# Optimization experiments

Hardware: AMD Instinct MI355X
Metric: run time of the kernel (lower is better)

The kernel has to match this reference:

```python
import jax, jax.numpy as jnp
import numpy as np

B, D, M = 32, 640, 1024
EPS = 1e-05


def setup_inputs() -> dict:
    key = jax.random.key(0)
    x = jax.random.normal(key, (B, D, M), dtype=jnp.float32)
    return {"x": x}


def _triu_flat_indices(d):
    iu, ju = np.triu_indices(d)
    return jnp.asarray(iu * d + ju, dtype=jnp.int32)


def reference(x):
    b, d, m = x.shape
    # Gram matrix: x @ x^T  -> [b, d, d]
    x_pow2 = jnp.einsum('bim,bjm->bij', x, x)
    # I_M @ (x_pow2 * I) + (x_pow2 * I) @ I_M - 2*x_pow2
    # (x_pow2 * I) is diagonal, so ones-matrix bmm = broadcast of the diagonal.
    diag = jnp.diagonal(x_pow2, axis1=1, axis2=2)  # [b, d]
    dcov = diag[:, None, :] + diag[:, :, None] - 2.0 * x_pow2
    dcov = jnp.maximum(dcov, 0.0)
    # temperature param is built in-forward: exp(log(1/(2*d*m))) = 1/(2*d*m)
    temperature = 1.0 / (2.0 * d * m)
    dcov = jnp.sqrt(temperature * dcov + EPS)
    # Double centering: dcov @ I_M = row sums broadcast; I_M @ dcov = col sums.
    row_mean = dcov.sum(axis=2, keepdims=True) / d          # [b, d, 1]
    col_mean = dcov.sum(axis=1, keepdims=True) / d          # [b, 1, d]
    tot_mean = dcov.sum(axis=(1, 2), keepdims=True) / (d * d)
    t = dcov - row_mean - col_mean + tot_mean               # [b, d, d]
    # Triuvec: gather upper-triangular entries (incl. diagonal)
    flat_idx = _triu_flat_indices(d)                         # [d*(d+1)//2]
    y = t.reshape(b, d * d)[:, flat_idx]
    return y
```

## Files before the change

kernel.cpp:

```cpp
#include <hip/hip_runtime.h>

#define D_DIM 640
#define M_DIM 1024
#define B_DIM 32
#define BK 32
#define OUT_ROW 205120

typedef __bf16 bf16x8 __attribute__((ext_vector_type(8)));
typedef float f32x4 __attribute__((ext_vector_type(4)));

__device__ __forceinline__ unsigned short f2bf(float f) {
    union { float f; unsigned int u; } c; c.f = f;
    unsigned int u = c.u;
    unsigned int r = (u + 0x7fffu + ((u >> 16) & 1u)) >> 16;
    return (unsigned short)r;
}

__device__ __forceinline__ void gload_lds16(const unsigned short* g, unsigned short* l) {
    __builtin_amdgcn_global_load_lds(
        (const __attribute__((address_space(1))) unsigned int*)g,
        (__attribute__((address_space(3))) unsigned int*)l,
        16, 0, 0);
}

__device__ __forceinline__ float block_reduce_256(float s) {
    #pragma unroll
    for (int off = 32; off > 0; off >>= 1) s += __shfl_down(s, off, 64);
    __shared__ float red[4];
    if ((threadIdx.x & 63) == 0) red[threadIdx.x >> 6] = s;
    __syncthreads();
    return red[0] + red[1] + red[2] + red[3];
}

__global__ void cast_diag_kernel(const float* __restrict__ x,
                                 unsigned short* __restrict__ xb,
                                 float* __restrict__ diag,
                                 float* __restrict__ rowsum,
                                 float* __restrict__ tot) {
    const size_t row = blockIdx.x;
    const int t = threadIdx.x;
    const float4 v = ((const float4*)(x + row * M_DIM))[t];
    float s = v.x * v.x + v.y * v.y + v.z * v.z + v.w * v.w;
    ushort4 o;
    o.x = f2bf(v.x); o.y = f2bf(v.y); o.z = f2bf(v.z); o.w = f2bf(v.w);
    ((ushort4*)(xb + row * M_DIM))[t] = o;
    float ssum = block_reduce_256(s);
    if (t == 0) { diag[row] = ssum; rowsum[row] = 0.f; }
    if (t == 1 && row < B_DIM) tot[row] = 0.f;
}

__global__ __launch_bounds__(256, 2)
void gemm_dcov_kernel(const unsigned short* __restrict__ xb,
                      const float* __restrict__ diag,
                      float* __restrict__ dcov,
                      float* __restrict__ rowsum,
                      float* __restrict__ tot) {
    __shared__ __align__(16) unsigned short smem[2 * 128 * BK];
    unsigned short* sA = smem;
    unsigned short* sB = smem + 128 * BK;

    int p = blockIdx.x, bt = blockIdx.y;
    int it = 0, off = p;
    while (off >= 5 - it) { off -= 5 - it; ++it; }
    const int jt = it + off;
    const bool diagTile = (it == jt);

    const int tid = threadIdx.x;
    const int w = tid >> 6, l = tid & 63;
    const int wy = w >> 1, wx = w & 1;
    const int lm = l & 15, quad = l >> 4;

    const unsigned short* gA = xb + ((size_t)bt * D_DIM + it * 128) * M_DIM;
    const unsigned short* gB = xb + ((size_t)bt * D_DIM + jt * 128) * M_DIM;

    const int r0 = tid >> 2;
    const int cl = (((tid & 3) ^ ((tid >> 3) & 3)) << 3);
    const size_t aoff1 = (size_t)r0 * M_DIM + cl;
    const size_t aoff2 = (size_t)(r0 + 64) * M_DIM + cl;
    const int ldst = tid * 8;

    f32x4 acc[4][4];
    const f32x4 zero = {0.f, 0.f, 0.f, 0.f};
    #pragma unroll
    for (int i = 0; i < 4; i++)
        #pragma unroll
        for (int j = 0; j < 4; j++) acc[i][j] = zero;

    const int sw = ((quad ^ ((lm >> 1) & 3)) << 3);

    for (int k0 = 0; k0 < M_DIM; k0 += BK) {
        gload_lds16(gA + aoff1 + k0, sA + ldst);
        gload_lds16(gA + aoff2 + k0, sA + ldst + 64 * BK);
        if (!diagTile) {
            gload_lds16(gB + aoff1 + k0, sB + ldst);
            gload_lds16(gB + aoff2 + k0, sB + ldst + 64 * BK);
        }
        __syncthreads();

        const unsigned short* sBB = diagTile ? sA : sB;
        bf16x8 af[4], bfr[4];
        #pragma unroll
        for (int mi = 0; mi < 4; mi++)
            af[mi] = *(const bf16x8*)&sA[(wy * 64 + mi * 16 + lm) * BK + sw];
        #pragma unroll
        for (int ni = 0; ni < 4; ni++)
            bfr[ni] = *(const bf16x8*)&sBB[(wx * 64 + ni * 16 + lm) * BK + sw];

        #pragma unroll
        for (int mi = 0; mi < 4; mi++)
            #pragma unroll
            for (int ni = 0; ni < 4; ni++)
                acc[mi][ni] = __builtin_amdgcn_mfma_f32_16x16x32_bf16(
                    af[mi], bfr[ni], acc[mi][ni], 0, 0, 0);
        __syncthreads();
    }

    float* sd = (float*)smem;
    if (tid < 128) sd[tid] = diag[(size_t)bt * D_DIM + it * 128 + tid];
    else           sd[tid] = diag[(size_t)bt * D_DIM + jt * 128 + (tid - 128)];
    __syncthreads();

    const float temp = 7.62939453125e-07f;
    float* dbase = dcov + (size_t)bt * D_DIM * D_DIM;
    float* rs = rowsum + (size_t)bt * D_DIM;
    float ts = 0.f;
    float cp[4] = {0.f, 0.f, 0.f, 0.f};

    #pragma unroll
    for (int mi = 0; mi < 4; mi++) {
        #pragma unroll
        for (int r = 0; r < 4; r++) {
            const int lrow = wy * 64 + mi * 16 + quad * 4 + r;
            const int grow = it * 128 + lrow;
            const float di = sd[lrow];
            float rp = 0.f;
            #pragma unroll
            for (int ni = 0; ni < 4; ni++) {
                const int lcol = wx * 64 + ni * 16 + lm;
                const int gcol = jt * 128 + lcol;
                const float dj = sd[128 + lcol];
                const float g = acc[mi][ni][r];
                const float v = sqrtf(fmaf(temp, fmaxf(di + dj - 2.f * g, 0.f), 1e-5f));
                dbase[(size_t)grow * D_DIM + gcol] = v;
                rp += v;
                cp[ni] += v;
            }
            ts += rp;
            rp += __shfl_down(rp, 8, 16);
            rp += __shfl_down(rp, 4, 16);
            rp += __shfl_down(rp, 2, 16);
            rp += __shfl_down(rp, 1, 16);
            if (lm == 0) atomicAdd(&rs[grow], rp);
        }
    }
    if (!diagTile) {
        #pragma unroll
        for (int ni = 0; ni < 4; ni++) {
            float c = cp[ni];
            c += __shfl_down(c, 32);
            c += __shfl_down(c, 16);
            if (l < 16) atomicAdd(&rs[jt * 128 + wx * 64 + ni * 16 + lm], c);
        }
    }
    float bs = block_reduce_256(ts);
    if (tid == 0) atomicAdd(&tot[bt], diagTile ? bs : 2.f * bs);
}

__global__ void output_kernel(const float* __restrict__ dcov,
                              const float* __restrict__ rowsum,
                              const float* __restrict__ tot,
                              float* __restrict__ out) {
    const int b = blockIdx.x / D_DIM;
    const int i = blockIdx.x - b * D_DIM;
    const float inv_d = 1.f / (float)D_DIM;
    const float rmi = rowsum[(size_t)b * D_DIM + i] * inv_d;
    const float tm = tot[b] * (inv_d * inv_d);
    const float* drow = dcov + ((size_t)b * D_DIM + i) * D_DIM;
    const float* rs = rowsum + (size_t)b * D_DIM;
    float* orow = out + (size_t)b * OUT_ROW + (size_t)i * D_DIM - (size_t)i * (i - 1) / 2;
    for (int j = i + threadIdx.x; j < D_DIM; j += 256)
        orow[j - i] = drow[j] - rmi - rs[j] * inv_d + tm;
}

extern "C" void kernel_launch(void* const* d_in, const int* in_sizes, int n_in,
                              void* d_out, int out_size, void* d_ws, size_t ws_size,
                              hipStream_t stream) {
    const float* x = (const float*)d_in[0];
    float* out = (float*)d_out;

    char* ws = (char*)d_ws;
    unsigned short* xb = (unsigned short*)ws;
    size_t off = 41943040;
    float* diag = (float*)(ws + off);   off += 81920;
    float* dcov = (float*)(ws + off);   off += 52428800;
    float* rowsum = (float*)(ws + off); off += 81920;
    float* tot = (float*)(ws + off);    off += 256;

    cast_diag_kernel<<<dim3(B_DIM * D_DIM), 256, 0, stream>>>(x, xb, diag, rowsum, tot);
    gemm_dcov_kernel<<<dim3(15, B_DIM), 256, 0, stream>>>(xb, diag, dcov, rowsum, tot);
    output_kernel<<<dim3(B_DIM * D_DIM), 256, 0, stream>>>(dcov, rowsum, tot, out);
}
```

Measured before the change: 184.7 us.

## Triple-buffer LDS loads in Gram GEMM and remap blocks across batches

Replaces the single-buffered load-sync-compute loop in the GEMM with a three-stage LDS ring. Loads run three k-steps ahead and are gated by explicit vmcnt waits and raw s_barrier instead of __syncthreads. The grid is flattened to 1D and block ids are remapped so consecutive blocks spread over batches, which likely aims to balance work across XCDs and caches. Diagonal tiles now load B separately instead of reusing A, adding redundant traffic, and the hand-written waitcnt logic depends on the exact count of in-flight loads.

```diff
diff --git a/kernel.cpp b/kernel.cpp
--- a/kernel.cpp
+++ b/kernel.cpp
@@ -55,11 +55,11 @@
                       float* __restrict__ dcov,
                       float* __restrict__ rowsum,
                       float* __restrict__ tot) {
-    __shared__ __align__(16) unsigned short smem[2 * 128 * BK];
-    unsigned short* sA = smem;
-    unsigned short* sB = smem + 128 * BK;
-
-    int p = blockIdx.x, bt = blockIdx.y;
+    __shared__ __align__(16) unsigned short smem[24576];
+
+    const int id = blockIdx.x;
+    const int bt = (id & 7) * 4 + ((id >> 3) & 3);
+    int p = id >> 5;
     int it = 0, off = p;
     while (off >= 5 - it) { off -= 5 - it; ++it; }
     const int jt = it + off;
@@ -76,8 +76,18 @@
     const int r0 = tid >> 2;
     const int cl = (((tid & 3) ^ ((tid >> 3) & 3)) << 3);
     const size_t aoff1 = (size_t)r0 * M_DIM + cl;
-    const size_t aoff2 = (size_t)(r0 + 64) * M_DIM + cl;
+    const size_t aoff2 = aoff1 + (size_t)64 * M_DIM;
     const int ldst = tid * 8;
+
+    auto issue = [&](int k, int ph) {
+        unsigned short* sA = smem + ph * 8192;
+        unsigned short* sB = sA + 4096;
+        const int koff = k * BK;
+        gload_lds16(gA + aoff1 + koff, sA + ldst);
+        gload_lds16(gA + aoff2 + koff, sA + ldst + 2048);
+        gload_lds16(gB + aoff1 + koff, sB + ldst);
+        gload_lds16(gB + aoff2 + koff, sB + ldst + 2048);
+    };
 
     f32x4 acc[4][4];
     const f32x4 zero = {0.f, 0.f, 0.f, 0.f};
@@ -88,23 +98,24 @@
 
     const int sw = ((quad ^ ((lm >> 1) & 3)) << 3);
 
-    for (int k0 = 0; k0 < M_DIM; k0 += BK) {
-        gload_lds16(gA + aoff1 + k0, sA + ldst);
-        gload_lds16(gA + aoff2 + k0, sA + ldst + 64 * BK);
-        if (!diagTile) {
-            gload_lds16(gB + aoff1 + k0, sB + ldst);
-            gload_lds16(gB + aoff2 + k0, sB + ldst + 64 * BK);
-        }
-        __syncthreads();
-
-        const unsigned short* sBB = diagTile ? sA : sB;
+    issue(0, 0); issue(1, 1); issue(2, 2);
+
+    int ph = 0;
+    for (int k = 0; k < 32; ++k) {
+        if (k < 30)       asm volatile("s_waitcnt vmcnt(8)" ::: "memory");
+        else if (k == 30) asm volatile("s_waitcnt vmcnt(4)" ::: "memory");
+        else              asm volatile("s_waitcnt vmcnt(0)" ::: "memory");
+        asm volatile("s_barrier" ::: "memory");
+
+        const unsigned short* sA = smem + ph * 8192;
+        const unsigned short* sB = sA + 4096;
         bf16x8 af[4], bfr[4];
         #pragma unroll
         for (int mi = 0; mi < 4; mi++)
             af[mi] = *(const bf16x8*)&sA[(wy * 64 + mi * 16 + lm) * BK + sw];
         #pragma unroll
         for (int ni = 0; ni < 4; ni++)
-            bfr[ni] = *(const bf16x8*)&sBB[(wx * 64 + ni * 16 + lm) * BK + sw];
+            bfr[ni] = *(const bf16x8*)&sB[(wx * 64 + ni * 16 + lm) * BK + sw];
 
         #pragma unroll
         for (int mi = 0; mi < 4; mi++)
@@ -112,7 +123,10 @@
             for (int ni = 0; ni < 4; ni++)
                 acc[mi][ni] = __builtin_amdgcn_mfma_f32_16x16x32_bf16(
                     af[mi], bfr[ni], acc[mi][ni], 0, 0, 0);
-        __syncthreads();
+
+        asm volatile("s_barrier" ::: "memory");
+        if (k + 3 < 32) issue(k + 3, ph);
+        ph = (ph == 2) ? 0 : ph + 1;
     }
 
     float* sd = (float*)smem;
@@ -197,6 +211,6 @@
     float* tot = (float*)(ws + off);    off += 256;
 
     cast_diag_kernel<<<dim3(B_DIM * D_DIM), 256, 0, stream>>>(x, xb, diag, rowsum, tot);
-    gemm_dcov_kernel<<<dim3(15, B_DIM), 256, 0, stream>>>(xb, diag, dcov, rowsum, tot);
+    gemm_dcov_kernel<<<dim3(480), 256, 0, stream>>>(xb, diag, dcov, rowsum, tot);
     output_kernel<<<dim3(B_DIM * D_DIM), 256, 0, stream>>>(dcov, rowsum, tot, out);
 }
```

Result: faster. 175.7 us (-4.9%).
